# Kernel tuning notes

Measured on AMD Instinct MI355X. Metric: run time of the kernel, lower is better.

## Reference

```python
import jax, jax.numpy as jnp
import numpy as np

B, C, QK, T, S = 16, 256, 32, 15, 31


def _conv1x1(x, w, b):
    # 1x1 conv as channel matmul; w: [out, in]
    return jnp.einsum("oc,bchw->bohw", w, x) + b[None, :, None, None]


def _spatial_attn(x, qw, qb, kw, kb, vw, vb, g):
    Bn, Cn, H, W = x.shape
    N = H * W
    q = _conv1x1(x, qw, qb).reshape(Bn, -1, N)  # [B,QK,N]
    k = _conv1x1(x, kw, kb).reshape(Bn, -1, N)  # [B,QK,N]
    v = _conv1x1(x, vw, vb).reshape(Bn, Cn, N)  # [B,C,N]
    energy = jnp.einsum("bqn,bqm->bnm", q, k)   # [B,N,N]
    A = jax.nn.softmax(energy, axis=-1)
    out = g * jnp.einsum("bcm,bnm->bcn", v, A)
    return out.reshape(Bn, Cn, H, W)


def _channel_attn_calc(x):
    Bn, Cn = x.shape[0], x.shape[1]
    f = x.reshape(Bn, Cn, -1)
    e = jnp.einsum("bcn,bdn->bcd", f, f)  # [B,C,C]
    e = jnp.max(e, axis=-1, keepdims=True) - e
    return jax.nn.softmax(e, axis=-1)


def _channel_attn_use(x, A, w):
    Bn, Cn = x.shape[0], x.shape[1]
    v = x.reshape(Bn, Cn, -1)
    return (w * jnp.einsum("bcd,bdn->bcn", A, v)).reshape(x.shape)


def _mod_deform_conv(x, ow, ob, w, b):
    # Modulated deformable conv (DCNv2) 3x3, pad 1, stride 1.
    Bn, Cn, H, W = x.shape
    om = jax.lax.conv_general_dilated(x, ow, (1, 1), ((1, 1), (1, 1)),
                                      dimension_numbers=("NCHW", "OIHW", "NCHW"))
    om = om + ob[None, :, None, None]  # [B,27,H,W]
    off_y, off_x, mask = om[:, :9], om[:, 9:18], jax.nn.sigmoid(om[:, 18:])
    ky, kx = jnp.meshgrid(jnp.arange(3), jnp.arange(3), indexing="ij")
    py = off_y + jnp.arange(H)[None, None, :, None] + (ky.reshape(9) - 1)[None, :, None, None]
    px = off_x + jnp.arange(W)[None, None, None, :] + (kx.reshape(9) - 1)[None, :, None, None]
    y0f = jnp.floor(py); x0f = jnp.floor(px)
    wy = py - y0f; wx = px - x0f
    y0 = y0f.astype(jnp.int32); x0 = x0f.astype(jnp.int32)
    xf = x.reshape(Bn, Cn, H * W)

    def gather(yi, xi, wgt):
        valid = (yi >= 0) & (yi < H) & (xi >= 0) & (xi < W)
        idx = (jnp.clip(yi, 0, H - 1) * W + jnp.clip(xi, 0, W - 1)).reshape(Bn, -1)
        g = jax.vmap(lambda a, i: a[:, i])(xf, idx).reshape(Bn, Cn, 9, H, W)
        return g * (wgt * valid.astype(x.dtype))[:, None]

    val = (gather(y0, x0, (1 - wy) * (1 - wx)) + gather(y0, x0 + 1, (1 - wy) * wx)
           + gather(y0 + 1, x0, wy * (1 - wx)) + gather(y0 + 1, x0 + 1, wy * wx))
    val = val * mask[:, None]  # [B,C,9,H,W]
    return jnp.einsum("bckhw,ock->bohw", val, w.reshape(w.shape[0], Cn, 9)) + b[None, :, None, None]


def _forward(template_features, sr_features,
             t_sp_qw, t_sp_qb, t_sp_kw, t_sp_kb, t_sp_vw, t_sp_vb, t_sp_g,
             s_sp_qw, s_sp_qb, s_sp_kw, s_sp_kb, s_sp_vw, s_sp_vb, s_sp_g,
             w_t_ch, w_s_ch, w_s2t, w_t2s,
             t_off_w, t_off_b, t_dcn_w, t_dcn_b,
             s_off_w, s_off_b, s_dcn_w, s_dcn_b):
    t, s = template_features, sr_features
    t_sp = _spatial_attn(t, t_sp_qw, t_sp_qb, t_sp_kw, t_sp_kb, t_sp_vw, t_sp_vb, t_sp_g)
    s_sp = _spatial_attn(s, s_sp_qw, s_sp_qb, s_sp_kw, s_sp_kb, s_sp_vw, s_sp_vb, s_sp_g)
    tA = _channel_attn_calc(t)
    sA = _channel_attn_calc(s)
    t_ch = _channel_attn_use(t, tA, w_t_ch)
    s_ch = _channel_attn_use(s, sA, w_s_ch)
    t_x = _channel_attn_use(t, sA, w_s2t)   # sr->template cross attention
    s_x = _channel_attn_use(s, tA, w_t2s)   # template->sr cross attention
    t_out = t + t_sp + t_ch + t_x
    s_out = s + s_sp + s_ch + s_x
    t_out = _mod_deform_conv(t_out, t_off_w, t_off_b, t_dcn_w, t_dcn_b)
    s_out = _mod_deform_conv(s_out, s_off_w, s_off_b, s_dcn_w, s_dcn_b)
    return t_out, s_out


def setup_inputs() -> dict:
    key = jax.random.key(0)
    ks = jax.random.split(key, 28)
    r = lambda i, shape, sc=0.05: jax.random.normal(ks[i], shape, dtype=jnp.float32) * sc
    return {
        "template_features": jax.random.normal(ks[0], (B, C, T, T), dtype=jnp.float32),
        "sr_features": jax.random.normal(ks[1], (B, C, S, S), dtype=jnp.float32),
        "t_sp_qw": r(2, (QK, C)), "t_sp_qb": r(3, (QK,)),
        "t_sp_kw": r(4, (QK, C)), "t_sp_kb": r(5, (QK,)),
        "t_sp_vw": r(6, (C, C)), "t_sp_vb": r(7, (C,)), "t_sp_g": r(8, (1,), 0.5),
        "s_sp_qw": r(9, (QK, C)), "s_sp_qb": r(10, (QK,)),
        "s_sp_kw": r(11, (QK, C)), "s_sp_kb": r(12, (QK,)),
        "s_sp_vw": r(13, (C, C)), "s_sp_vb": r(14, (C,)), "s_sp_g": r(15, (1,), 0.5),
        "w_t_ch": r(16, (1,), 0.5), "w_s_ch": r(17, (1,), 0.5),
        "w_s2t": r(18, (1,), 0.5), "w_t2s": r(19, (1,), 0.5),
        "t_off_w": r(20, (27, C, 3, 3), 0.01), "t_off_b": r(21, (27,), 0.01),
        "t_dcn_w": r(22, (C, C, 3, 3)), "t_dcn_b": r(23, (C,)),
        "s_off_w": r(24, (27, C, 3, 3), 0.01), "s_off_b": r(25, (27,), 0.01),
        "s_dcn_w": r(26, (C, C, 3, 3)), "s_dcn_b": r(27, (C,)),
    }


def reference(template_features, sr_features,
              t_sp_qw, t_sp_qb, t_sp_kw, t_sp_kb, t_sp_vw, t_sp_vb, t_sp_g,
              s_sp_qw, s_sp_qb, s_sp_kw, s_sp_kb, s_sp_vw, s_sp_vb, s_sp_g,
              w_t_ch, w_s_ch, w_s2t, w_t2s,
              t_off_w, t_off_b, t_dcn_w, t_dcn_b,
              s_off_w, s_off_b, s_dcn_w, s_dcn_b):
    return _forward(template_features, sr_features,
                    t_sp_qw, t_sp_qb, t_sp_kw, t_sp_kb, t_sp_vw, t_sp_vb, t_sp_g,
                    s_sp_qw, s_sp_qb, s_sp_kw, s_sp_kb, s_sp_vw, s_sp_vb, s_sp_g,
                    w_t_ch, w_s_ch, w_s2t, w_t2s,
                    t_off_w, t_off_b, t_dcn_w, t_dcn_b,
                    s_off_w, s_off_b, s_dcn_w, s_dcn_b)
```

## Files before the change

### kernel.cpp

```cpp
#include <hip/hip_runtime.h>
#include <hip/hip_bf16.h>
#include <cmath>

typedef __attribute__((ext_vector_type(8))) short bf16x8;
typedef __attribute__((ext_vector_type(4))) float f32x4;

__device__ inline ushort f2bf(float f) {
  __hip_bfloat16 h = __float2bfloat16(f);
  return *reinterpret_cast<ushort*>(&h);
}
__device__ inline float bf2f(ushort u) {
  return __uint_as_float((uint)u << 16);
}
__device__ inline float bflo(uint x) { return __uint_as_float(x << 16); }
__device__ inline float bfhi(uint x) { return __uint_as_float(x & 0xffff0000u); }

__device__ inline bool fdecode(int totalS, int gxS, int gyS, int gxT, int gyT,
                               int& bx, int& by, int& bz, bool& isT) {
  const int total = gridDim.x;
  const int id = blockIdx.x;
  int wid = (id & 7) * (total >> 3) + (id >> 3);
  const int totalT = gxT * gyT * 16;
  if (wid >= totalS + totalT) return false;
  isT = wid >= totalS;
  int lid = isT ? wid - totalS : wid;
  const int gx = isT ? gxT : gxS;
  const int gy = isT ? gyT : gyS;
  bx = lid % gx;
  lid /= gx;
  by = lid % gy;
  bz = lid / gy;
  return true;
}

__device__ inline void vdecode(int v, int vtotal, int totalS, int gxS, int gyS,
                               int gxT, int gyT, int& bx, int& by, int& bz,
                               bool& isT) {
  int wid = (v & 7) * (vtotal >> 3) + (v >> 3);
  isT = wid >= totalS;
  int lid = isT ? wid - totalS : wid;
  const int gx = isT ? gxT : gxS;
  const int gy = isT ? gyT : gyS;
  bx = lid % gx;
  lid /= gx;
  by = lid % gy;
  bz = lid / gy;
}

__global__ __launch_bounds__(256) void prep_cast_fused_kernel(
    const float* __restrict__ t_qw, const float* __restrict__ t_qb,
    const float* __restrict__ t_kw, const float* __restrict__ t_kb,
    const float* __restrict__ s_qw, const float* __restrict__ s_qb,
    const float* __restrict__ s_kw, const float* __restrict__ s_kb,
    const float* __restrict__ t_vw, const float* __restrict__ t_vb,
    const float* __restrict__ s_vw, const float* __restrict__ s_vb,
    const float* __restrict__ t_off_w, const float* __restrict__ s_off_w,
    const float* __restrict__ t_dcn_w, const float* __restrict__ s_dcn_w,
    ushort* __restrict__ Wall_t, ushort* __restrict__ Wall_s,
    float* __restrict__ biasAll_t, float* __restrict__ biasAll_s,
    ushort* __restrict__ owb_t, ushort* __restrict__ owb_s,
    ushort* __restrict__ Awb_t, ushort* __restrict__ Awb_s,
    const float* __restrict__ xS, ushort* __restrict__ oS,
    ushort* __restrict__ pS, int NS_, int NRS_, int NpS_,
    const float* __restrict__ xT, ushort* __restrict__ oT,
    ushort* __restrict__ pT, int NT_, int NRT_, int NpT_,
    float* __restrict__ rsS, float* __restrict__ rsT) {
  __shared__ float T[64][65];
  const int tid = threadIdx.x;
  const int vid = blockIdx.x;
  if (vid < 5832) {
    int i = vid * 256 + tid;
    if (i < 81920) {
      const int r = i >> 8, c = i & 255;
      float v;
      if (r < 256) v = t_vw[(size_t)r * 256 + c];
      else if (r < 288) v = t_qw[(size_t)(r - 256) * 256 + c];
      else v = t_kw[(size_t)(r - 288) * 256 + c];
      Wall_t[i] = f2bf(v);
      return;
    }
    i -= 81920;
    if (i < 81920) {
      const int r = i >> 8, c = i & 255;
      float v;
      if (r < 256) v = s_vw[(size_t)r * 256 + c];
      else if (r < 288) v = s_qw[(size_t)(r - 256) * 256 + c];
      else v = s_kw[(size_t)(r - 288) * 256 + c];
      Wall_s[i] = f2bf(v);
      return;
    }
    i -= 81920;
    if (i < 320) {
      biasAll_t[i] = (i < 256) ? t_vb[i] : ((i < 288) ? t_qb[i - 256] : t_kb[i - 288]);
      return;
    }
    i -= 320;
    if (i < 320) {
      biasAll_s[i] = (i < 256) ? s_vb[i] : ((i < 288) ? s_qb[i - 256] : s_kb[i - 288]);
      return;
    }
    i -= 320;
    if (i < 73728) {
      const int o = i / 2304, k = i % 2304, tap = k >> 8, c = k & 255;
      owb_t[i] = (o < 27) ? f2bf(t_off_w[(size_t)o * 2304 + c * 9 + tap]) : (ushort)0;
      return;
    }
    i -= 73728;
    if (i < 73728) {
      const int o = i / 2304, k = i % 2304, tap = k >> 8, c = k & 255;
      owb_s[i] = (o < 27) ? f2bf(s_off_w[(size_t)o * 2304 + c * 9 + tap]) : (ushort)0;
      return;
    }
    i -= 73728;
    if (i < 589824) {
      const int frag = i >> 9, within = i & 511;
      const int lane = within >> 3, j = within & 7;
      const int mt = frag / 72, kt = frag % 72;
      const int o = mt * 16 + (lane & 15);
      const int k = kt * 32 + (lane >> 4) * 8 + j;
      const int tap = k >> 8, c = k & 255;
      Awb_t[i] = f2bf(t_dcn_w[(size_t)o * 2304 + c * 9 + tap]);
      return;
    }
    i -= 589824;
    if (i < 589824) {
      const int frag = i >> 9, within = i & 511;
      const int lane = within >> 3, j = within & 7;
      const int mt = frag / 72, kt = frag % 72;
      const int o = mt * 16 + (lane & 15);
      const int k = kt * 32 + (lane >> 4) * 8 + j;
      const int tap = k >> 8, c = k & 255;
      Awb_s[i] = f2bf(s_dcn_w[(size_t)o * 2304 + c * 9 + tap]);
    }
    return;
  }
  if (vid >= 7112) {
    int i = (vid - 7112) * 256 + tid;
    if (i < 15376) rsS[i] = 0.f;
    else if (i < 18976) rsT[i - 15376] = 0.f;
    return;
  }
  constexpr int C = 256;
  int bx, by, bz; bool isT;
  vdecode(vid - 5832, 1280, 1024, 16, 4, 4, 4, bx, by, bz, isT);
  const float* x = isT ? xT : xS;
  ushort* xTo = isT ? oT : oS;
  ushort* xbf = isT ? pT : pS;
  const int N = isT ? NT_ : NS_;
  const int NR = isT ? NRT_ : NRS_;
  const int Np = isT ? NpT_ : NpS_;
  const int b = bz;
  const int n0 = bx * 64, c0 = by * 64;
  const float* xb = x + (size_t)b * C * N;
  for (int u = tid; u < 4096; u += 256) {
    const int cc = u >> 6, nn = u & 63;
    const int gn = n0 + nn;
    T[cc][nn] = (gn < N) ? xb[(size_t)(c0 + cc) * N + gn] : 0.f;
  }
  __syncthreads();
  ushort* ob = xTo + (size_t)b * NR * C;
  for (int u = tid; u < 4096; u += 256) {
    const int nn = u >> 6, cc = u & 63;
    ob[(size_t)(n0 + nn) * C + c0 + cc] = f2bf(T[cc][nn]);
  }
  ushort* pb = xbf + (size_t)b * C * Np;
  for (int u = tid; u < 4096; u += 256) {
    const int cc = u >> 6, nn = u & 63;
    const int gn = n0 + nn;
    if (gn < Np) pb[(size_t)(c0 + cc) * Np + gn] = f2bf(T[cc][nn]);
  }
}

__global__ __launch_bounds__(256) void proj_gram_fused_kernel(
    const ushort* __restrict__ WallS, const float* __restrict__ bS,
    const ushort* __restrict__ BtS, ushort* __restrict__ vS,
    float* __restrict__ qkS, int NS_, int NpS_, int NRS_,
    const ushort* __restrict__ WallT, const float* __restrict__ bT,
    const ushort* __restrict__ BtT, ushort* __restrict__ vT,
    float* __restrict__ qkT, int NT_, int NpT_, int NRT_,
    const ushort* __restrict__ xbfS, float* __restrict__ AscP, int KpS_,
    const ushort* __restrict__ xbfT, float* __restrict__ AtcP, int KpT_) {
  constexpr int C = 256;
  __shared__ ushort Asm[128][40];
  __shared__ ushort Bsm[64][40];
  const int tid = threadIdx.x, lane = tid & 63, w = tid >> 6;
  const int vid = blockIdx.x;
  if (vid < 1600) {
    int bx, by, bz; bool isT;
    vdecode(vid, 1600, 1280, 16, 5, 4, 5, bx, by, bz, isT);
    const ushort* Wall = isT ? WallT : WallS;
    const float* bias = isT ? bT : bS;
    const ushort* Bt = isT ? BtT : BtS;
    ushort* vbf = isT ? vT : vS;
    float* qk = isT ? qkT : qkS;
    const int N = isT ? NT_ : NS_, Np = isT ? NpT_ : NpS_, NR = isT ? NRT_ : NRS_;
    const int n0 = bx * 64, m0 = by * 64, b = bz;
    const ushort* Ab = Wall + (size_t)m0 * C;
    const ushort* Bb = Bt + (size_t)b * NR * C;
    f32x4 acc[4];
#pragma unroll
    for (int i = 0; i < 4; i++) acc[i] = (f32x4){0.f, 0.f, 0.f, 0.f};
    for (int k0 = 0; k0 < C; k0 += 32) {
      {
        const int row = tid >> 2, seg = tid & 3;
        *reinterpret_cast<uint4*>(&Asm[row][seg * 8]) =
            *reinterpret_cast<const uint4*>(&Ab[(size_t)row * C + k0 + seg * 8]);
        *reinterpret_cast<uint4*>(&Bsm[row][seg * 8]) =
            *reinterpret_cast<const uint4*>(&Bb[(size_t)(n0 + row) * C + k0 + seg * 8]);
      }
      __syncthreads();
      const int koff = (lane >> 4) * 8;
      const bf16x8 bfr = *reinterpret_cast<const bf16x8*>(&Bsm[w * 16 + (lane & 15)][koff]);
#pragma unroll
      for (int mf = 0; mf < 4; mf++) {
        const bf16x8 af = *reinterpret_cast<const bf16x8*>(&Asm[mf * 16 + (lane & 15)][koff]);
        acc[mf] = __builtin_amdgcn_mfma_f32_16x16x32_bf16(af, bfr, acc[mf], 0, 0, 0);
      }
      __syncthreads();
    }
    const int gn = n0 + w * 16 + (lane & 15);
#pragma unroll
    for (int mf = 0; mf < 4; mf++) {
      const int mbase = m0 + mf * 16 + ((lane >> 4) * 4);
#pragma unroll
      for (int rr = 0; rr < 4; rr++) {
        const int m = mbase + rr;
        if (m < 256) {
          if (gn < Np) {
            ushort v = (gn < N) ? f2bf(acc[mf][rr] + bias[m]) : (ushort)0;
            vbf[((size_t)b * 256 + m) * Np + gn] = v;
          }
        } else {
          if (gn < N)
            qk[((size_t)b * 64 + (m - 256)) * N + gn] = acc[mf][rr] + bias[m];
        }
      }
    }
    return;
  }
  {
    constexpr int BM = 128, NW = 4, NF = 2, WN = 2;
    int bx, by, bz; bool isT;
    vdecode(vid - 1600, 256, 128, 4, 2, 4, 2, bx, by, bz, isT);
    const ushort* A = isT ? xbfT : xbfS;
    float* outF = isT ? AtcP : AscP;
    const int Kp = isT ? KpT_ : KpS_;
    const int n0 = bx * 64, m0 = by * BM, b = bz;
    const ushort* Ab = A + (size_t)b * C * Kp;
    const int wr = w / WN, wc = w % WN;
    f32x4 acc[4][NF];
#pragma unroll
    for (int i = 0; i < 4; i++)
#pragma unroll
      for (int j = 0; j < NF; j++) acc[i][j] = (f32x4){0.f, 0.f, 0.f, 0.f};
    for (int k0 = 0; k0 < Kp; k0 += 32) {
      for (int u = tid; u < BM * 4; u += NW * 64) {
        const int row = u >> 2, seg = u & 3;
        *reinterpret_cast<uint4*>(&Asm[row][seg * 8]) =
            *reinterpret_cast<const uint4*>(&Ab[(size_t)(m0 + row) * Kp + k0 + seg * 8]);
      }
      for (int u = tid; u < 64 * 4; u += NW * 64) {
        const int row = u >> 2, seg = u & 3;
        *reinterpret_cast<uint4*>(&Bsm[row][seg * 8]) =
            *reinterpret_cast<const uint4*>(&Ab[(size_t)(n0 + row) * Kp + k0 + seg * 8]);
      }
      __syncthreads();
      const int koff = (lane >> 4) * 8;
      bf16x8 af[4], bfr[NF];
#pragma unroll
      for (int mf = 0; mf < 4; mf++)
        af[mf] = *reinterpret_cast<const bf16x8*>(&Asm[wr * 64 + mf * 16 + (lane & 15)][koff]);
#pragma unroll
      for (int nf = 0; nf < NF; nf++)
        bfr[nf] = *reinterpret_cast<const bf16x8*>(&Bsm[wc * NF * 16 + nf * 16 + (lane & 15)][koff]);
#pragma unroll
      for (int mf = 0; mf < 4; mf++)
#pragma unroll
        for (int nf = 0; nf < NF; nf++)
          acc[mf][nf] = __builtin_amdgcn_mfma_f32_16x16x32_bf16(af[mf], bfr[nf], acc[mf][nf], 0, 0, 0);
      __syncthreads();
    }
#pragma unroll
    for (int mf = 0; mf < 4; mf++) {
      const int mbase = m0 + wr * 64 + mf * 16 + ((lane >> 4) * 4);
#pragma unroll
      for (int nf = 0; nf < NF; nf++) {
        const int gn = n0 + wc * NF * 16 + nf * 16 + (lane & 15);
#pragma unroll
        for (int rr = 0; rr < 4; rr++)
          outF[((size_t)b * C + mbase + rr) * C + gn] = acc[mf][nf][rr];
      }
    }
  }
}

__global__ __launch_bounds__(256) void energy_mcomb_fused_kernel(
    const float* __restrict__ qkS, ushort* __restrict__ SS, int NS_, int NpS_,
    const float* __restrict__ qkT, ushort* __restrict__ ST, int NT_, int NpT_,
    float* __restrict__ rsS, float* __restrict__ rsT,
    const float* __restrict__ Atc, const float* __restrict__ Asc,
    const float* __restrict__ w_t_ch, const float* __restrict__ w_s2t,
    const float* __restrict__ w_s_ch, const float* __restrict__ w_t2s,
    ushort* __restrict__ Mc_t, ushort* __restrict__ Mc_s) {
  __shared__ ushort Aq[64][40];
  __shared__ ushort Bk[64][40];
  __shared__ float red[8];
  const int tid = threadIdx.x;
  const int vid = blockIdx.x;
  if (vid < 4352) {
    int bx, by, bz; bool isT;
    vdecode(vid, 4352, 4096, 16, 16, 4, 4, bx, by, bz, isT);
    const float* qk = isT ? qkT : qkS;
    ushort* Sbf = isT ? ST : SS;
    float* rowsum = isT ? rsT : rsS;
    const int N = isT ? NT_ : NS_, Np = isT ? NpT_ : NpS_;
    const int m0 = bx * 64, n0 = by * 64, b = bz;
    const float* qb = qk + (size_t)b * 64 * N;
    const float* kb = qb + (size_t)32 * N;
    const int lane = tid & 63, w = tid >> 6;
    for (int u = tid; u < 2048; u += 256) {
      const int c = u >> 6, nn = u & 63;
      const int gn = n0 + nn, gm = m0 + nn;
      Aq[nn][c] = (gn < N) ? f2bf(qb[(size_t)c * N + gn]) : (ushort)0;
      Bk[nn][c] = (gm < N) ? f2bf(kb[(size_t)c * N + gm]) : (ushort)0;
    }
    __syncthreads();
    const int koff = (lane >> 4) * 8;
    const bf16x8 af = *reinterpret_cast<const bf16x8*>(&Aq[w * 16 + (lane & 15)][koff]);
    f32x4 acc[4];
#pragma unroll
    for (int j = 0; j < 4; j++) {
      const bf16x8 bf = *reinterpret_cast<const bf16x8*>(&Bk[j * 16 + (lane & 15)][koff]);
      acc[j] = __builtin_amdgcn_mfma_f32_16x16x32_bf16(af, bf, (f32x4){0.f, 0.f, 0.f, 0.f}, 0, 0, 0);
    }
    float psum[4] = {0.f, 0.f, 0.f, 0.f};
#pragma unroll
    for (int j = 0; j < 4; j++) {
      const int m = m0 + j * 16 + (lane & 15);
#pragma unroll
      for (int r = 0; r < 4; r++) {
        const int n = n0 + w * 16 + (lane >> 4) * 4 + r;
        float e = 0.f;
        if (m < N) e = __expf(acc[j][r]);
        if (m < Np && n < N) Sbf[((size_t)b * N + n) * Np + m] = f2bf(e);
        psum[r] += e;
      }
    }
#pragma unroll
    for (int d = 1; d < 16; d <<= 1) {
#pragma unroll
      for (int r = 0; r < 4; r++) psum[r] += __shfl_xor(psum[r], d, 64);
    }
    if ((lane & 15) == 0) {
#pragma unroll
      for (int r = 0; r < 4; r++) {
        const int n = n0 + w * 16 + (lane >> 4) * 4 + r;
        if (n < N) atomicAdd(&rowsum[(size_t)b * N + n], psum[r]);
      }
    }
    return;
  }
  {
    const int row = vid - 4352;
    const size_t idx = (size_t)row * 256 + tid;
    const float a = -Atc[idx];
    const float s = -Asc[idx];
    float ma = a, ms = s;
#pragma unroll
    for (int off = 32; off; off >>= 1) {
      ma = fmaxf(ma, __shfl_xor(ma, off, 64));
      ms = fmaxf(ms, __shfl_xor(ms, off, 64));
    }
    if ((tid & 63) == 0) { red[tid >> 6] = ma; red[4 + (tid >> 6)] = ms; }
    __syncthreads();
    if (tid == 0) {
      float m1 = red[0], m2 = red[4];
      for (int i = 1; i < 4; i++) { m1 = fmaxf(m1, red[i]); m2 = fmaxf(m2, red[4 + i]); }
      red[0] = m1; red[4] = m2;
    }
    __syncthreads();
    ma = red[0]; ms = red[4];
    __syncthreads();
    const float ea = __expf(a - ma), es = __expf(s - ms);
    float sa = ea, ss = es;
#pragma unroll
    for (int off = 32; off; off >>= 1) {
      sa += __shfl_xor(sa, off, 64);
      ss += __shfl_xor(ss, off, 64);
    }
    if ((tid & 63) == 0) { red[tid >> 6] = sa; red[4 + (tid >> 6)] = ss; }
    __syncthreads();
    if (tid == 0) {
      float t1 = 0.f, t2 = 0.f;
      for (int i = 0; i < 4; i++) { t1 += red[i]; t2 += red[4 + i]; }
      red[0] = t1; red[4] = t2;
    }
    __syncthreads();
    const float Pa = ea / red[0], Ps = es / red[4];
    Mc_t[idx] = f2bf(w_t_ch[0] * Pa + w_s2t[0] * Ps);
    Mc_s[idx] = f2bf(w_s_ch[0] * Ps + w_t2s[0] * Pa);
  }
}

__global__ __launch_bounds__(256) void pv_chan_fused_kernel(
    const ushort* __restrict__ vS, const ushort* __restrict__ SS,
    const float* __restrict__ rsS, const ushort* __restrict__ McS,
    const ushort* __restrict__ xTS, const float* __restrict__ xS,
    const float* __restrict__ gS, ushort* __restrict__ xsTS, int NS_,
    int NpS_, int NRS_,
    const ushort* __restrict__ vT, const ushort* __restrict__ ST,
    const float* __restrict__ rsT, const ushort* __restrict__ McT,
    const ushort* __restrict__ xTT, const float* __restrict__ xT_,
    const float* __restrict__ gT, ushort* __restrict__ xsTT, int NT_,
    int NpT_, int NRT_) {
  constexpr int C = 256, BM = 128, NW = 4, NF = 2, WN = 2;
  __shared__ ushort Asm[BM][40];
  __shared__ ushort Bsm[64][40];
  int bx, by, bz; bool isT;
  if (!fdecode(512, 16, 2, 4, 2, bx, by, bz, isT)) return;
  const ushort* vbf = isT ? vT : vS;
  const ushort* Sbf = isT ? ST : SS;
  const float* rowsum = isT ? rsT : rsS;
  const ushort* Mc = isT ? McT : McS;
  const ushort* xTb = isT ? xTT : xTS;
  const float* x = isT ? xT_ : xS;
  const float* gp = isT ? gT : gS;
  ushort* xsT = isT ? xsTT : xsTS;
  const int N = isT ? NT_ : NS_, Np = isT ? NpT_ : NpS_;
  const int NR = isT ? NRT_ : NRS_;
  const int n0 = bx * 64, m0 = by * BM, b = bz;
  const int tid = threadIdx.x, lane = tid & 63, w = tid >> 6;
  const int wr = w / WN, wc = w % WN;
  f32x4 acc[4][NF];
#pragma unroll
  for (int i = 0; i < 4; i++)
#pragma unroll
    for (int j = 0; j < NF; j++) acc[i][j] = (f32x4){0.f, 0.f, 0.f, 0.f};
  const int koff = (lane >> 4) * 8;
  {
    const ushort* Ab = vbf + (size_t)b * C * Np;
    const ushort* Bb = Sbf + (size_t)b * (size_t)N * Np;
    for (int k0 = 0; k0 < Np; k0 += 32) {
      for (int u = tid; u < BM * 4; u += NW * 64) {
        const int row = u >> 2, seg = u & 3;
        *reinterpret_cast<uint4*>(&Asm[row][seg * 8]) =
            *reinterpret_cast<const uint4*>(&Ab[(size_t)(m0 + row) * Np + k0 + seg * 8]);
      }
      for (int u = tid; u < 64 * 4; u += NW * 64) {
        const int row = u >> 2, seg = u & 3;
        const int gn = n0 + row;
        uint4 val;
        if (gn < N)
          val = *reinterpret_cast<const uint4*>(&Bb[(size_t)gn * Np + k0 + seg * 8]);
        else
          val = make_uint4(0, 0, 0, 0);
        *reinterpret_cast<uint4*>(&Bsm[row][seg * 8]) = val;
      }
      __syncthreads();
      bf16x8 af[4], bfr[NF];
#pragma unroll
      for (int mf = 0; mf < 4; mf++)
        af[mf] = *reinterpret_cast<const bf16x8*>(&Asm[wr * 64 + mf * 16 + (lane & 15)][koff]);
#pragma unroll
      for (int nf = 0; nf < NF; nf++)
        bfr[nf] = *reinterpret_cast<const bf16x8*>(&Bsm[wc * NF * 16 + nf * 16 + (lane & 15)][koff]);
#pragma unroll
      for (int mf = 0; mf < 4; mf++)
#pragma unroll
        for (int nf = 0; nf < NF; nf++)
          acc[mf][nf] = __builtin_amdgcn_mfma_f32_16x16x32_bf16(af[mf], bfr[nf], acc[mf][nf], 0, 0, 0);
      __syncthreads();
    }
  }
  const float g = *gp;
  float fac[NF];
#pragma unroll
  for (int nf = 0; nf < NF; nf++) {
    const int gn = n0 + wc * NF * 16 + nf * 16 + (lane & 15);
    const float rs = (gn < N) ? rowsum[(size_t)b * N + gn] : 1.f;
    fac[nf] = g / rs;
  }
#pragma unroll
  for (int mf = 0; mf < 4; mf++)
#pragma unroll
    for (int nf = 0; nf < NF; nf++)
#pragma unroll
      for (int rr = 0; rr < 4; rr++) acc[mf][nf][rr] *= fac[nf];
  {
    const ushort* Ab = Mc + (size_t)b * C * C;
    const ushort* Bb = xTb + (size_t)b * NR * C;
    for (int k0 = 0; k0 < C; k0 += 32) {
      for (int u = tid; u < BM * 4; u += NW * 64) {
        const int row = u >> 2, seg = u & 3;
        *reinterpret_cast<uint4*>(&Asm[row][seg * 8]) =
            *reinterpret_cast<const uint4*>(&Ab[(size_t)(m0 + row) * C + k0 + seg * 8]);
      }
      for (int u = tid; u < 64 * 4; u += NW * 64) {
        const int row = u >> 2, seg = u & 3;
        *reinterpret_cast<uint4*>(&Bsm[row][seg * 8]) =
            *reinterpret_cast<const uint4*>(&Bb[(size_t)(n0 + row) * C + k0 + seg * 8]);
      }
      __syncthreads();
      bf16x8 af[4], bfr[NF];
#pragma unroll
      for (int mf = 0; mf < 4; mf++)
        af[mf] = *reinterpret_cast<const bf16x8*>(&Asm[wr * 64 + mf * 16 + (lane & 15)][koff]);
#pragma unroll
      for (int nf = 0; nf < NF; nf++)
        bfr[nf] = *reinterpret_cast<const bf16x8*>(&Bsm[wc * NF * 16 + nf * 16 + (lane & 15)][koff]);
#pragma unroll
      for (int mf = 0; mf < 4; mf++)
#pragma unroll
        for (int nf = 0; nf < NF; nf++)
          acc[mf][nf] = __builtin_amdgcn_mfma_f32_16x16x32_bf16(af[mf], bfr[nf], acc[mf][nf], 0, 0, 0);
      __syncthreads();
    }
  }
#pragma unroll
  for (int mf = 0; mf < 4; mf++) {
    const int mbase = m0 + wr * 64 + mf * 16 + ((lane >> 4) * 4);
#pragma unroll
    for (int nf = 0; nf < NF; nf++) {
      const int gn = n0 + wc * NF * 16 + nf * 16 + (lane & 15);
      if (gn < N) {
        float s[4];
#pragma unroll
        for (int rr = 0; rr < 4; rr++)
          s[rr] = x[((size_t)b * C + mbase + rr) * N + gn] + acc[mf][nf][rr];
        uint lo = (uint)f2bf(s[0]) | ((uint)f2bf(s[1]) << 16);
        uint hi = (uint)f2bf(s[2]) | ((uint)f2bf(s[3]) << 16);
        *reinterpret_cast<uint2*>(&xsT[((size_t)b * NR + gn) * C + mbase]) =
            make_uint2(lo, hi);
      }
    }
  }
}

__global__ __launch_bounds__(256) void offconv_prep_fused_kernel(
    const ushort* __restrict__ xS, const ushort* __restrict__ owS,
    const float* __restrict__ obS, uint4* __restrict__ prS, int HS_, int WS_,
    int NS_, int NRS_,
    const ushort* __restrict__ xT, const ushort* __restrict__ owT,
    const float* __restrict__ obT, uint4* __restrict__ prT, int HT_, int WT_,
    int NT_, int NRT_) {
  __shared__ ushort Asm[32][136];
  __shared__ ushort Bsm[64][136];
  __shared__ int qsrc[64];
  __shared__ float som[27][65];
  int bx, by, bz; bool isT;
  if (!fdecode(256, 16, 1, 4, 1, bx, by, bz, isT)) return;
  const ushort* xsT = isT ? xT : xS;
  const ushort* owb = isT ? owT : owS;
  const float* ob = isT ? obT : obS;
  uint4* prep = isT ? prT : prS;
  const int H = isT ? HT_ : HS_, Wd = isT ? WT_ : WS_;
  const int N = isT ? NT_ : NS_, NR = isT ? NRT_ : NRS_;
  const int n0 = bx * 64, b = bz;
  const int tid = threadIdx.x, lane = tid & 63, w = tid >> 6;
  const ushort* xb = xsT + (size_t)b * NR * 256;
  f32x4 acc[2];
  acc[0] = (f32x4){0.f, 0.f, 0.f, 0.f};
  acc[1] = (f32x4){0.f, 0.f, 0.f, 0.f};
  for (int tap = 0; tap < 9; ++tap) {
    const int dy = tap / 3 - 1, dx = tap - (tap / 3) * 3 - 1;
    if (tid < 64) {
      const int p = n0 + tid;
      int q = -1;
      if (p < N) {
        const int h = p / Wd, ww = p - (p / Wd) * Wd;
        const int yy = h + dy, xx = ww + dx;
        if (yy >= 0 && yy < H && xx >= 0 && xx < Wd) q = yy * Wd + xx;
      }
      qsrc[tid] = q;
    }
    __syncthreads();
#pragma unroll
    for (int half = 0; half < 2; ++half) {
      const int k0 = tap * 256 + half * 128;
      for (int u = tid; u < 512; u += 256) {
        const int row = u >> 4, seg = u & 15;
        *reinterpret_cast<uint4*>(&Asm[row][seg * 8]) =
            *reinterpret_cast<const uint4*>(&owb[(size_t)row * 2304 + k0 + seg * 8]);
      }
      for (int u = tid; u < 1024; u += 256) {
        const int row = u >> 4, seg = u & 15;
        const int q = qsrc[row];
        uint4 val = make_uint4(0, 0, 0, 0);
        if (q >= 0)
          val = *reinterpret_cast<const uint4*>(&xb[(size_t)q * 256 + half * 128 + seg * 8]);
        *reinterpret_cast<uint4*>(&Bsm[row][seg * 8]) = val;
      }
      __syncthreads();
#pragma unroll
      for (int sub = 0; sub < 4; ++sub) {
        const int koff = sub * 32 + (lane >> 4) * 8;
        const bf16x8 b0 = *reinterpret_cast<const bf16x8*>(&Bsm[w * 16 + (lane & 15)][koff]);
#pragma unroll
        for (int mf = 0; mf < 2; ++mf) {
          const bf16x8 a0 = *reinterpret_cast<const bf16x8*>(&Asm[mf * 16 + (lane & 15)][koff]);
          acc[mf] = __builtin_amdgcn_mfma_f32_16x16x32_bf16(a0, b0, acc[mf], 0, 0, 0);
        }
      }
      __syncthreads();
    }
  }
#pragma unroll
  for (int mf = 0; mf < 2; ++mf) {
#pragma unroll
    for (int r = 0; r < 4; ++r) {
      const int o = mf * 16 + (lane >> 4) * 4 + r;
      const int n = w * 16 + (lane & 15);
      if (o < 27) som[o][n] = acc[mf][r] + ob[o];
    }
  }
  __syncthreads();
  for (int u = tid; u < 576; u += 256) {
    const int tap = u / 64, pp = u - (u / 64) * 64;
    const int p = n0 + pp;
    if (p >= N) continue;
    const float offy = som[tap][pp];
    const float offx = som[9 + tap][pp];
    const float mraw = som[18 + tap][pp];
    const float mval = 1.f / (1.f + __expf(-mraw));
    const int ky = tap / 3, kx = tap - (tap / 3) * 3;
    const int h = p / Wd, ww = p - (p / Wd) * Wd;
    const float py = offy + (float)(h + ky - 1);
    const float px = offx + (float)(ww + kx - 1);
    const float y0f = floorf(py), x0f = floorf(px);
    const float wy = py - y0f, wx = px - x0f;
    const int y0 = (int)y0f, x0 = (int)x0f;
    const int ys0 = min(max(y0, 0), H - 2);
    const int xs0 = min(max(x0, 0), Wd - 2);
    const float wr0 = (ys0 == y0) ? (1.f - wy) : ((ys0 == y0 + 1) ? wy : 0.f);
    const float wr1 = (ys0 + 1 == y0) ? (1.f - wy) : ((ys0 + 1 == y0 + 1) ? wy : 0.f);
    const float wc0 = (xs0 == x0) ? (1.f - wx) : ((xs0 == x0 + 1) ? wx : 0.f);
    const float wc1 = (xs0 + 1 == x0) ? (1.f - wx) : ((xs0 + 1 == x0 + 1) ? wx : 0.f);
    const float w00 = wr0 * wc0 * mval, w01 = wr0 * wc1 * mval;
    const float w10 = wr1 * wc0 * mval, w11 = wr1 * wc1 * mval;
    uint4 pk;
    pk.x = (uint)(ys0 * Wd + xs0);
    pk.y = (uint)f2bf(w00) | ((uint)f2bf(w01) << 16);
    pk.z = (uint)f2bf(w10) | ((uint)f2bf(w11) << 16);
    pk.w = 0;
    prep[((size_t)b * 9 + tap) * N + p] = pk;
  }
}

__global__ __launch_bounds__(512) void dcn_fused_kernel(
    const ushort* __restrict__ xS, const uint4* __restrict__ prS,
    const ushort* __restrict__ AwS, const float* __restrict__ biS,
    float* __restrict__ oS, int NS_, int WS_, int NRS_,
    const ushort* __restrict__ xT, const uint4* __restrict__ prT,
    const ushort* __restrict__ AwT, const float* __restrict__ biT,
    float* __restrict__ oT, int NT_, int WT_, int NRT_) {
  constexpr int C = 256, MF = 4;
  __shared__ ushort Bsm[32][72];
  __shared__ int sq[32];
  __shared__ float swl[4][32];
  int bx, by, bz; bool isT;
  if (!fdecode(512, 32, 1, 8, 1, bx, by, bz, isT)) return;
  const ushort* xsT = isT ? xT : xS;
  const uint4* prep = isT ? prT : prS;
  const ushort* Awb = isT ? AwT : AwS;
  const float* bias = isT ? biT : biS;
  float* out = isT ? oT : oS;
  const int N = isT ? NT_ : NS_, Wd = isT ? WT_ : WS_, NR = isT ? NRT_ : NRS_;
  const int n0 = bx * 32, b = bz;
  const int tid = threadIdx.x, lane = tid & 63, w = tid >> 6;
  const int wr = w >> 1, wc = w & 1;
  const ushort* xb = xsT + (size_t)b * NR * C;
  const int un0 = tid >> 5;
  const int un1 = un0 + 16;
  const int kk2 = (tid & 31) * 2;
  f32x4 acc[MF];
#pragma unroll
  for (int i = 0; i < MF; i++) acc[i] = (f32x4){0.f, 0.f, 0.f, 0.f};
  uint bReg[2][4];
  int sqr0 = 0, sqr1 = 0;
  float w0a[4], w1a[4];
  const size_t rowYp = (size_t)Wd * C;
  for (int tap = 0; tap < 9; ++tap) {
    if (tid < 32) {
      const int p = n0 + tid;
      if (p < N) {
        const uint4 pk = prep[((size_t)b * 9 + tap) * N + p];
        sq[tid] = (int)pk.x * C;
        swl[0][tid] = bf2f((ushort)(pk.y & 0xffff));
        swl[1][tid] = bf2f((ushort)(pk.y >> 16));
        swl[2][tid] = bf2f((ushort)(pk.z & 0xffff));
        swl[3][tid] = bf2f((ushort)(pk.z >> 16));
      } else {
        sq[tid] = 0;
        swl[0][tid] = swl[1][tid] = swl[2][tid] = swl[3][tid] = 0.f;
      }
    }
    __syncthreads();
    sqr0 = sq[un0];
    sqr1 = sq[un1];
#pragma unroll
    for (int q = 0; q < 4; q++) {
      w0a[q] = swl[q][un0];
      w1a[q] = swl[q][un1];
    }
    {
      const ushort* pA = xb + sqr0 + kk2;
      bReg[0][0] = *reinterpret_cast<const uint*>(pA);
      bReg[0][1] = *reinterpret_cast<const uint*>(pA + C);
      bReg[0][2] = *reinterpret_cast<const uint*>(pA + rowYp);
      bReg[0][3] = *reinterpret_cast<const uint*>(pA + rowYp + C);
      const ushort* pB = xb + sqr1 + kk2;
      bReg[1][0] = *reinterpret_cast<const uint*>(pB);
      bReg[1][1] = *reinterpret_cast<const uint*>(pB + C);
      bReg[1][2] = *reinterpret_cast<const uint*>(pB + rowYp);
      bReg[1][3] = *reinterpret_cast<const uint*>(pB + rowYp + C);
    }
#pragma unroll
    for (int ks = 0; ks < 4; ++ks) {
      bf16x8 afr[2][4];
      const int ktb = tap * 8 + ks * 2;
#pragma unroll
      for (int sub = 0; sub < 2; ++sub)
#pragma unroll
        for (int mf = 0; mf < 4; ++mf)
          afr[sub][mf] = *reinterpret_cast<const bf16x8*>(
              Awb + ((((size_t)(wr * 4 + mf) * 72) + ktb + sub) << 9) + lane * 8);
      {
        const float vlo0 = w0a[0] * bflo(bReg[0][0]) + w0a[1] * bflo(bReg[0][1]) +
                           w0a[2] * bflo(bReg[0][2]) + w0a[3] * bflo(bReg[0][3]);
        const float vhi0 = w0a[0] * bfhi(bReg[0][0]) + w0a[1] * bfhi(bReg[0][1]) +
                           w0a[2] * bfhi(bReg[0][2]) + w0a[3] * bfhi(bReg[0][3]);
        *reinterpret_cast<uint*>(&Bsm[un0][kk2]) =
            (uint)f2bf(vlo0) | ((uint)f2bf(vhi0) << 16);
        const float vlo1 = w1a[0] * bflo(bReg[1][0]) + w1a[1] * bflo(bReg[1][1]) +
                           w1a[2] * bflo(bReg[1][2]) + w1a[3] * bflo(bReg[1][3]);
        const float vhi1 = w1a[0] * bfhi(bReg[1][0]) + w1a[1] * bfhi(bReg[1][1]) +
                           w1a[2] * bfhi(bReg[1][2]) + w1a[3] * bfhi(bReg[1][3]);
        *reinterpret_cast<uint*>(&Bsm[un1][kk2]) =
            (uint)f2bf(vlo1) | ((uint)f2bf(vhi1) << 16);
      }
      __syncthreads();
      if (ks < 3) {
        const int c1 = (ks + 1) * 64;
        const ushort* pA = xb + sqr0 + c1 + kk2;
        bReg[0][0] = *reinterpret_cast<const uint*>(pA);
        bReg[0][1] = *reinterpret_cast<const uint*>(pA + C);
        bReg[0][2] = *reinterpret_cast<const uint*>(pA + rowYp);
        bReg[0][3] = *reinterpret_cast<const uint*>(pA + rowYp + C);
        const ushort* pB = xb + sqr1 + c1 + kk2;
        bReg[1][0] = *reinterpret_cast<const uint*>(pB);
        bReg[1][1] = *reinterpret_cast<const uint*>(pB + C);
        bReg[1][2] = *reinterpret_cast<const uint*>(pB + rowYp);
        bReg[1][3] = *reinterpret_cast<const uint*>(pB + rowYp + C);
      }
#pragma unroll
      for (int sub = 0; sub < 2; ++sub) {
        const int koff = sub * 32 + (lane >> 4) * 8;
        const bf16x8 bfv = *reinterpret_cast<const bf16x8*>(&Bsm[wc * 16 + (lane & 15)][koff]);
#pragma unroll
        for (int mf = 0; mf < MF; mf++)
          acc[mf] = __builtin_amdgcn_mfma_f32_16x16x32_bf16(afr[sub][mf], bfv, acc[mf], 0, 0, 0);
      }
      __syncthreads();
    }
  }
  const int gn = n0 + wc * 16 + (lane & 15);
#pragma unroll
  for (int mf = 0; mf < MF; mf++) {
    const int mbase = wr * 64 + mf * 16 + ((lane >> 4) * 4);
    if (gn < N) {
#pragma unroll
      for (int rr = 0; rr < 4; rr++)
        out[((size_t)b * C + mbase + rr) * N + gn] = acc[mf][rr] + bias[mbase + rr];
    }
  }
}

extern "C" void kernel_launch(void* const* d_in, const int* in_sizes, int n_in,
                              void* d_out, int out_size, void* d_ws, size_t ws_size,
                              hipStream_t stream) {
  const float* t_in = (const float*)d_in[0];
  const float* s_in = (const float*)d_in[1];
  const float* t_qw = (const float*)d_in[2];
  const float* t_qb = (const float*)d_in[3];
  const float* t_kw = (const float*)d_in[4];
  const float* t_kb = (const float*)d_in[5];
  const float* t_vw = (const float*)d_in[6];
  const float* t_vb = (const float*)d_in[7];
  const float* t_g = (const float*)d_in[8];
  const float* s_qw = (const float*)d_in[9];
  const float* s_qb = (const float*)d_in[10];
  const float* s_kw = (const float*)d_in[11];
  const float* s_kb = (const float*)d_in[12];
  const float* s_vw = (const float*)d_in[13];
  const float* s_vb = (const float*)d_in[14];
  const float* s_g = (const float*)d_in[15];
  const float* w_t_ch = (const float*)d_in[16];
  const float* w_s_ch = (const float*)d_in[17];
  const float* w_s2t = (const float*)d_in[18];
  const float* w_t2s = (const float*)d_in[19];
  const float* t_off_w = (const float*)d_in[20];
  const float* t_off_b = (const float*)d_in[21];
  const float* t_dcn_w = (const float*)d_in[22];
  const float* t_dcn_b = (const float*)d_in[23];
  const float* s_off_w = (const float*)d_in[24];
  const float* s_off_b = (const float*)d_in[25];
  const float* s_dcn_w = (const float*)d_in[26];
  const float* s_dcn_b = (const float*)d_in[27];
  (void)in_sizes; (void)n_in; (void)out_size; (void)ws_size;

  constexpr int Bn = 16, C = 256;
  constexpr int HT = 15, WT = 15, NT = HT * WT;
  constexpr int HS = 31, WS2 = 31, NS = HS * WS2;
  constexpr int NpT = 256, NpS = 992;
  constexpr int NRT = 256, NRS = 1024;

  float* ws = (float*)d_ws;
  size_t off = 0;
  auto alloc = [&](size_t n) {
    n = (n + 3) & ~(size_t)3;
    float* p = ws + off; off += n; return p;
  };
  auto allocU = [&](size_t nu) { return (ushort*)alloc((nu + 1) / 2); };

  float* qk_t = alloc((size_t)Bn * 64 * NT);
  float* qk_s = alloc((size_t)Bn * 64 * NS);
  ushort* Wall_t = allocU((size_t)320 * C);
  ushort* Wall_s = allocU((size_t)320 * C);
  float* biasAll_t = alloc(320);
  float* biasAll_s = alloc(320);
  ushort* xT_t = allocU((size_t)Bn * NRT * C);
  ushort* xT_s = allocU((size_t)Bn * NRS * C);
  ushort* xbf_t = allocU((size_t)Bn * C * NpT);
  ushort* xbf_s = allocU((size_t)Bn * C * NpS);
  ushort* v_tbf = allocU((size_t)Bn * C * NpT);
  ushort* v_sbf = allocU((size_t)Bn * C * NpS);
  ushort* S_t = allocU((size_t)Bn * NT * NpT);
  ushort* S_s = allocU((size_t)Bn * NS * NpS);
  float* rs_t = alloc((size_t)Bn * NT);
  float* rs_s = alloc((size_t)Bn * NS);
  ushort* xsT_t = allocU((size_t)Bn * NRT * C);
  ushort* xsT_s = allocU((size_t)Bn * NRS * C);
  float* Atc = alloc((size_t)Bn * C * C);
  float* Asc = alloc((size_t)Bn * C * C);
  ushort* Mc_t = allocU((size_t)Bn * C * C);
  ushort* Mc_s = allocU((size_t)Bn * C * C);
  ushort* owb_t = allocU((size_t)32 * 2304);
  ushort* owb_s = allocU((size_t)32 * 2304);
  ushort* Awb_t = allocU((size_t)256 * 2304);
  ushort* Awb_s = allocU((size_t)256 * 2304);
  uint4* prep_t = (uint4*)alloc((size_t)Bn * 9 * NT * 4);
  uint4* prep_s = (uint4*)alloc((size_t)Bn * 9 * NS * 4);

  dim3 blk(256);

  prep_cast_fused_kernel<<<dim3(5832 + 1280 + 75), blk, 0, stream>>>(
      t_qw, t_qb, t_kw, t_kb, s_qw, s_qb, s_kw, s_kb,
      t_vw, t_vb, s_vw, s_vb, t_off_w, s_off_w, t_dcn_w, s_dcn_w,
      Wall_t, Wall_s, biasAll_t, biasAll_s, owb_t, owb_s, Awb_t, Awb_s,
      s_in, xT_s, xbf_s, NS, NRS, NpS, t_in, xT_t, xbf_t, NT, NRT, NpT,
      rs_s, rs_t);

  proj_gram_fused_kernel<<<dim3(1600 + 256), blk, 0, stream>>>(
      Wall_s, biasAll_s, xT_s, v_sbf, qk_s, NS, NpS, NRS,
      Wall_t, biasAll_t, xT_t, v_tbf, qk_t, NT, NpT, NRT,
      xbf_s, Asc, NpS, xbf_t, Atc, NpT);

  energy_mcomb_fused_kernel<<<dim3(4352 + 4096), blk, 0, stream>>>(
      qk_s, S_s, NS, NpS, qk_t, S_t, NT, NpT, rs_s, rs_t,
      Atc, Asc, w_t_ch, w_s2t, w_s_ch, w_t2s, Mc_t, Mc_s);

  pv_chan_fused_kernel<<<dim3(640), blk, 0, stream>>>(
      v_sbf, S_s, rs_s, Mc_s, xT_s, s_in, s_g, xsT_s, NS, NpS, NRS,
      v_tbf, S_t, rs_t, Mc_t, xT_t, t_in, t_g, xsT_t, NT, NpT, NRT);

  offconv_prep_fused_kernel<<<dim3(320), blk, 0, stream>>>(
      xsT_s, owb_s, s_off_b, prep_s, HS, WS2, NS, NRS,
      xsT_t, owb_t, t_off_b, prep_t, HT, WT, NT, NRT);

  float* out_t = (float*)d_out;
  float* out_s = out_t + (size_t)Bn * C * NT;
  dcn_fused_kernel<<<dim3(640), dim3(512), 0, stream>>>(
      xsT_s, prep_s, Awb_s, s_dcn_b, out_s, NS, WS2, NRS,
      xsT_t, prep_t, Awb_t, t_dcn_b, out_t, NT, WT, NRT);
}
```

Before: 256.7 us.

## Fuse spatial attention energy, softmax and PV into a flash-style kernel

Replaces the separate energy kernel, which wrote a full bf16 exp-score matrix plus atomic row sums, and the PV GEMM in the channel kernel with one flash-style kernel. For each 64-query tile and 128-channel slice it loops over key tiles, computes exp scores into shared memory and accumulates V·E with MFMA, then normalises by a locally reduced row sum and writes a bf16 PV result. This removes the large S matrix traffic, the rowsum zeroing and the atomics. In exchange the energy is recomputed once per channel slice, padding grows to 1024, and the grid drops to 640 blocks, so there is less parallelism.

```diff
diff --git a/kernel.cpp b/kernel.cpp
--- a/kernel.cpp
+++ b/kernel.cpp
@@ -63,8 +63,7 @@
     const float* __restrict__ xS, ushort* __restrict__ oS,
     ushort* __restrict__ pS, int NS_, int NRS_, int NpS_,
     const float* __restrict__ xT, ushort* __restrict__ oT,
-    ushort* __restrict__ pT, int NT_, int NRT_, int NpT_,
-    float* __restrict__ rsS, float* __restrict__ rsT) {
+    ushort* __restrict__ pT, int NT_, int NRT_, int NpT_) {
   __shared__ float T[64][65];
   const int tid = threadIdx.x;
   const int vid = blockIdx.x;
@@ -132,12 +131,6 @@
       const int tap = k >> 8, c = k & 255;
       Awb_s[i] = f2bf(s_dcn_w[(size_t)o * 2304 + c * 9 + tap]);
     }
-    return;
-  }
-  if (vid >= 7112) {
-    int i = (vid - 7112) * 256 + tid;
-    if (i < 15376) rsS[i] = 0.f;
-    else if (i < 18976) rsT[i - 15376] = 0.f;
     return;
   }
   constexpr int C = 256;
@@ -294,74 +287,129 @@
   }
 }
 
-__global__ __launch_bounds__(256) void energy_mcomb_fused_kernel(
-    const float* __restrict__ qkS, ushort* __restrict__ SS, int NS_, int NpS_,
-    const float* __restrict__ qkT, ushort* __restrict__ ST, int NT_, int NpT_,
-    float* __restrict__ rsS, float* __restrict__ rsT,
+__global__ __launch_bounds__(256) void flash_mcomb_fused_kernel(
+    const float* __restrict__ qkS, const ushort* __restrict__ vS,
+    const float* __restrict__ gS, ushort* __restrict__ pvS, int NS_, int NpS_,
+    const float* __restrict__ qkT, const ushort* __restrict__ vT,
+    const float* __restrict__ gT, ushort* __restrict__ pvT, int NT_, int NpT_,
     const float* __restrict__ Atc, const float* __restrict__ Asc,
     const float* __restrict__ w_t_ch, const float* __restrict__ w_s2t,
     const float* __restrict__ w_s_ch, const float* __restrict__ w_t2s,
     ushort* __restrict__ Mc_t, ushort* __restrict__ Mc_s) {
   __shared__ ushort Aq[64][40];
   __shared__ ushort Bk[64][40];
+  __shared__ ushort Es[64][72];
+  __shared__ float rsL[64];
   __shared__ float red[8];
   const int tid = threadIdx.x;
   const int vid = blockIdx.x;
-  if (vid < 4352) {
+  if (vid < 640) {
     int bx, by, bz; bool isT;
-    vdecode(vid, 4352, 4096, 16, 16, 4, 4, bx, by, bz, isT);
+    vdecode(vid, 640, 512, 16, 2, 4, 2, bx, by, bz, isT);
     const float* qk = isT ? qkT : qkS;
-    ushort* Sbf = isT ? ST : SS;
-    float* rowsum = isT ? rsT : rsS;
+    const ushort* vbf = isT ? vT : vS;
+    const float* gp = isT ? gT : gS;
+    ushort* pvb = isT ? pvT : pvS;
     const int N = isT ? NT_ : NS_, Np = isT ? NpT_ : NpS_;
-    const int m0 = bx * 64, n0 = by * 64, b = bz;
+    const int n0 = bx * 64, c0 = by * 128, b = bz;
     const float* qb = qk + (size_t)b * 64 * N;
     const float* kb = qb + (size_t)32 * N;
     const int lane = tid & 63, w = tid >> 6;
+    const int koffE = (lane >> 4) * 8;
     for (int u = tid; u < 2048; u += 256) {
       const int c = u >> 6, nn = u & 63;
-      const int gn = n0 + nn, gm = m0 + nn;
+      const int gn = n0 + nn;
       Aq[nn][c] = (gn < N) ? f2bf(qb[(size_t)c * N + gn]) : (ushort)0;
-      Bk[nn][c] = (gm < N) ? f2bf(kb[(size_t)c * N + gm]) : (ushort)0;
+    }
+    f32x4 acc[2][4];
+#pragma unroll
+    for (int i = 0; i < 2; i++)
+#pragma unroll
+      for (int j = 0; j < 4; j++) acc[i][j] = (f32x4){0.f, 0.f, 0.f, 0.f};
+    float psum[4] = {0.f, 0.f, 0.f, 0.f};
+    const int msteps = Np >> 6;
+    const size_t vrow0 = ((size_t)b * 256 + c0 + w * 32 + (lane & 15)) * Np;
+    for (int ms = 0; ms < msteps; ++ms) {
+      const int m0 = ms * 64;
+      for (int u = tid; u < 2048; u += 256) {
+        const int c = u >> 6, nn = u & 63;
+        const int gm = m0 + nn;
+        Bk[nn][c] = (gm < N) ? f2bf(kb[(size_t)c * N + gm]) : (ushort)0;
+      }
+      __syncthreads();
+      const bf16x8 afq = *reinterpret_cast<const bf16x8*>(&Aq[w * 16 + (lane & 15)][koffE]);
+      f32x4 eacc[4];
+#pragma unroll
+      for (int j = 0; j < 4; j++) {
+        const bf16x8 bfk = *reinterpret_cast<const bf16x8*>(&Bk[j * 16 + (lane & 15)][koffE]);
+        eacc[j] = __builtin_amdgcn_mfma_f32_16x16x32_bf16(afq, bfk, (f32x4){0.f, 0.f, 0.f, 0.f}, 0, 0, 0);
+      }
+#pragma unroll
+      for (int j = 0; j < 4; j++) {
+        const int mloc = j * 16 + (lane & 15);
+        const int gm = m0 + mloc;
+#pragma unroll
+        for (int r = 0; r < 4; r++) {
+          float e = (gm < N) ? __expf(eacc[j][r]) : 0.f;
+          Es[w * 16 + (lane >> 4) * 4 + r][mloc] = f2bf(e);
+          psum[r] += e;
+        }
+      }
+      __syncthreads();
+#pragma unroll
+      for (int sub = 0; sub < 2; ++sub) {
+        const int km = m0 + sub * 32 + koffE;
+        bf16x8 afv[2];
+#pragma unroll
+        for (int mf = 0; mf < 2; mf++)
+          afv[mf] = *reinterpret_cast<const bf16x8*>(&vbf[vrow0 + (size_t)mf * 16 * Np + km]);
+#pragma unroll
+        for (int nf = 0; nf < 4; nf++) {
+          const bf16x8 bfe = *reinterpret_cast<const bf16x8*>(&Es[nf * 16 + (lane & 15)][sub * 32 + koffE]);
+#pragma unroll
+          for (int mf = 0; mf < 2; mf++)
+            acc[mf][nf] = __builtin_amdgcn_mfma_f32_16x16x32_bf16(afv[mf], bfe, acc[mf][nf], 0, 0, 0);
+        }
+      }
+      __syncthreads();
+    }
+#pragma unroll
+    for (int d = 1; d < 16; d <<= 1) {
+#pragma unroll
+      for (int r = 0; r < 4; r++) psum[r] += __shfl_xor(psum[r], d, 64);
+    }
+    if ((lane & 15) == 0) {
+#pragma unroll
+      for (int r = 0; r < 4; r++) rsL[w * 16 + (lane >> 4) * 4 + r] = psum[r];
     }
     __syncthreads();
-    const int koff = (lane >> 4) * 8;
-    const bf16x8 af = *reinterpret_cast<const bf16x8*>(&Aq[w * 16 + (lane & 15)][koff]);
-    f32x4 acc[4];
-#pragma unroll
-    for (int j = 0; j < 4; j++) {
-      const bf16x8 bf = *reinterpret_cast<const bf16x8*>(&Bk[j * 16 + (lane & 15)][koff]);
-      acc[j] = __builtin_amdgcn_mfma_f32_16x16x32_bf16(af, bf, (f32x4){0.f, 0.f, 0.f, 0.f}, 0, 0, 0);
-    }
-    float psum[4] = {0.f, 0.f, 0.f, 0.f};
-#pragma unroll
-    for (int j = 0; j < 4; j++) {
-      const int m = m0 + j * 16 + (lane & 15);
-#pragma unroll
-      for (int r = 0; r < 4; r++) {
-        const int n = n0 + w * 16 + (lane >> 4) * 4 + r;
-        float e = 0.f;
-        if (m < N) e = __expf(acc[j][r]);
-        if (m < Np && n < N) Sbf[((size_t)b * N + n) * Np + m] = f2bf(e);
-        psum[r] += e;
-      }
-    }
-#pragma unroll
-    for (int d = 1; d < 16; d <<= 1) {
-#pragma unroll
-      for (int r = 0; r < 4; r++) psum[r] += __shfl_xor(psum[r], d, 64);
-    }
-    if ((lane & 15) == 0) {
-#pragma unroll
-      for (int r = 0; r < 4; r++) {
-        const int n = n0 + w * 16 + (lane >> 4) * 4 + r;
-        if (n < N) atomicAdd(&rowsum[(size_t)b * N + n], psum[r]);
+    const float g = *gp;
+    float fac[4];
+#pragma unroll
+    for (int nf = 0; nf < 4; nf++) {
+      const int nl = nf * 16 + (lane & 15);
+      fac[nf] = g / rsL[nl];
+    }
+#pragma unroll
+    for (int mf = 0; mf < 2; mf++) {
+      const int cb = c0 + w * 32 + mf * 16 + ((lane >> 4) * 4);
+#pragma unroll
+      for (int nf = 0; nf < 4; nf++) {
+        const int gn = n0 + nf * 16 + (lane & 15);
+        float v0 = acc[mf][nf][0] * fac[nf];
+        float v1 = acc[mf][nf][1] * fac[nf];
+        float v2 = acc[mf][nf][2] * fac[nf];
+        float v3 = acc[mf][nf][3] * fac[nf];
+        uint lo = (uint)f2bf(v0) | ((uint)f2bf(v1) << 16);
+        uint hi = (uint)f2bf(v2) | ((uint)f2bf(v3) << 16);
+        *reinterpret_cast<uint2*>(&pvb[((size_t)b * Np + gn) * 256 + cb]) =
+            make_uint2(lo, hi);
       }
     }
     return;
   }
   {
-    const int row = vid - 4352;
+    const int row = vid - 640;
     const size_t idx = (size_t)row * 256 + tid;
     const float a = -Atc[idx];
     const float s = -Asc[idx];
@@ -403,28 +451,21 @@
 }
 
 __global__ __launch_bounds__(256) void pv_chan_fused_kernel(
-    const ushort* __restrict__ vS, const ushort* __restrict__ SS,
-    const float* __restrict__ rsS, const ushort* __restrict__ McS,
+    const ushort* __restrict__ pvSb, const ushort* __restrict__ McS,
     const ushort* __restrict__ xTS, const float* __restrict__ xS,
-    const float* __restrict__ gS, ushort* __restrict__ xsTS, int NS_,
-    int NpS_, int NRS_,
-    const ushort* __restrict__ vT, const ushort* __restrict__ ST,
-    const float* __restrict__ rsT, const ushort* __restrict__ McT,
+    ushort* __restrict__ xsTS, int NS_, int NpS_, int NRS_,
+    const ushort* __restrict__ pvTb, const ushort* __restrict__ McT,
     const ushort* __restrict__ xTT, const float* __restrict__ xT_,
-    const float* __restrict__ gT, ushort* __restrict__ xsTT, int NT_,
-    int NpT_, int NRT_) {
+    ushort* __restrict__ xsTT, int NT_, int NpT_, int NRT_) {
   constexpr int C = 256, BM = 128, NW = 4, NF = 2, WN = 2;
   __shared__ ushort Asm[BM][40];
   __shared__ ushort Bsm[64][40];
   int bx, by, bz; bool isT;
   if (!fdecode(512, 16, 2, 4, 2, bx, by, bz, isT)) return;
-  const ushort* vbf = isT ? vT : vS;
-  const ushort* Sbf = isT ? ST : SS;
-  const float* rowsum = isT ? rsT : rsS;
+  const ushort* pvb = isT ? pvTb : pvSb;
   const ushort* Mc = isT ? McT : McS;
   const ushort* xTb = isT ? xTT : xTS;
   const float* x = isT ? xT_ : xS;
-  const float* gp = isT ? gT : gS;
   ushort* xsT = isT ? xsTT : xsTS;
   const int N = isT ? NT_ : NS_, Np = isT ? NpT_ : NpS_;
   const int NR = isT ? NRT_ : NRS_;
@@ -437,55 +478,6 @@
 #pragma unroll
     for (int j = 0; j < NF; j++) acc[i][j] = (f32x4){0.f, 0.f, 0.f, 0.f};
   const int koff = (lane >> 4) * 8;
-  {
-    const ushort* Ab = vbf + (size_t)b * C * Np;
-    const ushort* Bb = Sbf + (size_t)b * (size_t)N * Np;
-    for (int k0 = 0; k0 < Np; k0 += 32) {
-      for (int u = tid; u < BM * 4; u += NW * 64) {
-        const int row = u >> 2, seg = u & 3;
-        *reinterpret_cast<uint4*>(&Asm[row][seg * 8]) =
-            *reinterpret_cast<const uint4*>(&Ab[(size_t)(m0 + row) * Np + k0 + seg * 8]);
-      }
-      for (int u = tid; u < 64 * 4; u += NW * 64) {
-        const int row = u >> 2, seg = u & 3;
-        const int gn = n0 + row;
-        uint4 val;
-        if (gn < N)
-          val = *reinterpret_cast<const uint4*>(&Bb[(size_t)gn * Np + k0 + seg * 8]);
-        else
-          val = make_uint4(0, 0, 0, 0);
-        *reinterpret_cast<uint4*>(&Bsm[row][seg * 8]) = val;
-      }
-      __syncthreads();
-      bf16x8 af[4], bfr[NF];
-#pragma unroll
-      for (int mf = 0; mf < 4; mf++)
-        af[mf] = *reinterpret_cast<const bf16x8*>(&Asm[wr * 64 + mf * 16 + (lane & 15)][koff]);
-#pragma unroll
-      for (int nf = 0; nf < NF; nf++)
-        bfr[nf] = *reinterpret_cast<const bf16x8*>(&Bsm[wc * NF * 16 + nf * 16 + (lane & 15)][koff]);
-#pragma unroll
-      for (int mf = 0; mf < 4; mf++)
-#pragma unroll
-        for (int nf = 0; nf < NF; nf++)
-          acc[mf][nf] = __builtin_amdgcn_mfma_f32_16x16x32_bf16(af[mf], bfr[nf], acc[mf][nf], 0, 0, 0);
-      __syncthreads();
-    }
-  }
-  const float g = *gp;
-  float fac[NF];
-#pragma unroll
-  for (int nf = 0; nf < NF; nf++) {
-    const int gn = n0 + wc * NF * 16 + nf * 16 + (lane & 15);
-    const float rs = (gn < N) ? rowsum[(size_t)b * N + gn] : 1.f;
-    fac[nf] = g / rs;
-  }
-#pragma unroll
-  for (int mf = 0; mf < 4; mf++)
-#pragma unroll
-    for (int nf = 0; nf < NF; nf++)
-#pragma unroll
-      for (int rr = 0; rr < 4; rr++) acc[mf][nf][rr] *= fac[nf];
   {
     const ushort* Ab = Mc + (size_t)b * C * C;
     const ushort* Bb = xTb + (size_t)b * NR * C;
@@ -523,10 +515,13 @@
     for (int nf = 0; nf < NF; nf++) {
       const int gn = n0 + wc * NF * 16 + nf * 16 + (lane & 15);
       if (gn < N) {
+        const uint2 pvw = *reinterpret_cast<const uint2*>(
+            &pvb[((size_t)b * Np + gn) * 256 + mbase]);
         float s[4];
-#pragma unroll
-        for (int rr = 0; rr < 4; rr++)
-          s[rr] = x[((size_t)b * C + mbase + rr) * N + gn] + acc[mf][nf][rr];
+        s[0] = x[((size_t)b * C + mbase + 0) * N + gn] + bflo(pvw.x) + acc[mf][nf][0];
+        s[1] = x[((size_t)b * C + mbase + 1) * N + gn] + bfhi(pvw.x) + acc[mf][nf][1];
+        s[2] = x[((size_t)b * C + mbase + 2) * N + gn] + bflo(pvw.y) + acc[mf][nf][2];
+        s[3] = x[((size_t)b * C + mbase + 3) * N + gn] + bfhi(pvw.y) + acc[mf][nf][3];
         uint lo = (uint)f2bf(s[0]) | ((uint)f2bf(s[1]) << 16);
         uint hi = (uint)f2bf(s[2]) | ((uint)f2bf(s[3]) << 16);
         *reinterpret_cast<uint2*>(&xsT[((size_t)b * NR + gn) * C + mbase]) =
@@ -811,7 +806,7 @@
   constexpr int Bn = 16, C = 256;
   constexpr int HT = 15, WT = 15, NT = HT * WT;
   constexpr int HS = 31, WS2 = 31, NS = HS * WS2;
-  constexpr int NpT = 256, NpS = 992;
+  constexpr int NpT = 256, NpS = 1024;
   constexpr int NRT = 256, NRS = 1024;
 
   float* ws = (float*)d_ws;
@@ -834,10 +829,8 @@
   ushort* xbf_s = allocU((size_t)Bn * C * NpS);
   ushort* v_tbf = allocU((size_t)Bn * C * NpT);
   ushort* v_sbf = allocU((size_t)Bn * C * NpS);
-  ushort* S_t = allocU((size_t)Bn * NT * NpT);
-  ushort* S_s = allocU((size_t)Bn * NS * NpS);
-  float* rs_t = alloc((size_t)Bn * NT);
-  float* rs_s = alloc((size_t)Bn * NS);
+  ushort* pvb_t = allocU((size_t)Bn * NpT * C);
+  ushort* pvb_s = allocU((size_t)Bn * NpS * C);
   ushort* xsT_t = allocU((size_t)Bn * NRT * C);
   ushort* xsT_s = allocU((size_t)Bn * NRS * C);
   float* Atc = alloc((size_t)Bn * C * C);
@@ -853,25 +846,25 @@
 
   dim3 blk(256);
 
-  prep_cast_fused_kernel<<<dim3(5832 + 1280 + 75), blk, 0, stream>>>(
+  prep_cast_fused_kernel<<<dim3(5832 + 1280), blk, 0, stream>>>(
       t_qw, t_qb, t_kw, t_kb, s_qw, s_qb, s_kw, s_kb,
       t_vw, t_vb, s_vw, s_vb, t_off_w, s_off_w, t_dcn_w, s_dcn_w,
       Wall_t, Wall_s, biasAll_t, biasAll_s, owb_t, owb_s, Awb_t, Awb_s,
-      s_in, xT_s, xbf_s, NS, NRS, NpS, t_in, xT_t, xbf_t, NT, NRT, NpT,
-      rs_s, rs_t);
+      s_in, xT_s, xbf_s, NS, NRS, NpS, t_in, xT_t, xbf_t, NT, NRT, NpT);
 
   proj_gram_fused_kernel<<<dim3(1600 + 256), blk, 0, stream>>>(
       Wall_s, biasAll_s, xT_s, v_sbf, qk_s, NS, NpS, NRS,
       Wall_t, biasAll_t, xT_t, v_tbf, qk_t, NT, NpT, NRT,
       xbf_s, Asc, NpS, xbf_t, Atc, NpT);
 
-  energy_mcomb_fused_kernel<<<dim3(4352 + 4096), blk, 0, stream>>>(
-      qk_s, S_s, NS, NpS, qk_t, S_t, NT, NpT, rs_s, rs_t,
+  flash_mcomb_fused_kernel<<<dim3(640 + 4096), blk, 0, stream>>>(
+      qk_s, v_sbf, s_g, pvb_s, NS, NpS,
+      qk_t, v_tbf, t_g, pvb_t, NT, NpT,
       Atc, Asc, w_t_ch, w_s2t, w_s_ch, w_t2s, Mc_t, Mc_s);
 
   pv_chan_fused_kernel<<<dim3(640), blk, 0, stream>>>(
-      v_sbf, S_s, rs_s, Mc_s, xT_s, s_in, s_g, xsT_s, NS, NpS, NRS,
-      v_tbf, S_t, rs_t, Mc_t, xT_t, t_in, t_g, xsT_t, NT, NpT, NRT);
+      pvb_s, Mc_s, xT_s, s_in, xsT_s, NS, NpS, NRS,
+      pvb_t, Mc_t, xT_t, t_in, xsT_t, NT, NpT, NRT);
 
   offconv_prep_fused_kernel<<<dim3(320), blk, 0, stream>>>(
       xsT_s, owb_s, s_off_b, prep_s, HS, WS2, NS, NRS,
```

Measured after the change: 255.3 us, median of 2. No clear change (-0.5%).
